# Performance work log

Hardware: AMD Instinct MI355X
Metric: run time of the kernel (lower is better)

Reference implementation:

```python
import jax, jax.numpy as jnp
import numpy as np

# Face order: [+x, -x, +y, -y, +z, -z]

def _rot(v, face):
    # v: (B,3,nx,ny,nz) -> rotate into face-normal frame (rotate_vec_to_face_normal)
    vx, vy, vz = v[:, 0], v[:, 1], v[:, 2]
    if face == 0:  # +x
        return jnp.stack([vx, vy, vz], axis=1)
    if face == 1:  # -x
        return jnp.stack([-vx, vy, vz], axis=1)
    if face == 2:  # +y
        return jnp.stack([vy, vx, vz], axis=1)
    if face == 3:  # -y
        return jnp.stack([-vy, vx, vz], axis=1)
    if face == 4:  # +z
        return jnp.stack([vz, vx, vy], axis=1)
    return jnp.stack([-vz, vx, vy], axis=1)  # -z


def _neighbors(f):
    # f: (B,C,nx,ny,nz); x,y periodic, z non-periodic (zero pad)
    dst_px = jnp.roll(f, -1, axis=-3)
    dst_mx = jnp.roll(f, 1, axis=-3)
    dst_py = jnp.roll(f, -1, axis=-2)
    dst_my = jnp.roll(f, 1, axis=-2)
    z = jnp.zeros_like(f[..., :1])
    dst_pz = jnp.concatenate([f[..., 1:], z], axis=-1)
    dst_mz = jnp.concatenate([z, f[..., :-1]], axis=-1)
    return [dst_px, dst_mx, dst_py, dst_my, dst_pz, dst_mz]


def setup_inputs() -> dict:
    key = jax.random.key(0)
    ks = jax.random.split(key, 10)
    B, s, nx, ny, nz, H = 2, 8, 48, 48, 48, 64
    in_ch = 2 * (s + 5)   # 26
    out_ch = 4 + 5 * s    # 44
    counts = jax.random.uniform(ks[0], (B, s, nx, ny, nz), jnp.float32)
    momentum = jax.random.normal(ks[1], (B, 3, nx, ny, nz), jnp.float32)
    ke = jax.random.uniform(ks[2], (B, 1, nx, ny, nz), jnp.float32)
    order = jax.random.uniform(ks[3], (B, 1, nx, ny, nz), jnp.float32)

    def lin(k, o, i):
        k1, k2 = jax.random.split(k)
        lim = 1.0 / np.sqrt(i)
        W = jax.random.uniform(k1, (o, i), jnp.float32, -lim, lim)
        b = jax.random.uniform(k2, (o,), jnp.float32, -lim, lim)
        return W, b

    W1, b1 = lin(ks[4], H, in_ch)
    W2, b2 = lin(ks[5], H, H)
    W3, b3 = lin(ks[6], out_ch, H)
    return dict(counts=counts, momentum=momentum, ke=ke, order=order,
                W1=W1, b1=b1, W2=W2, b2=b2, W3=W3, b3=b3)


def reference(counts, momentum, ke, order, W1, b1, W2, b2, W3, b3):
    s = counts.shape[1]
    # state.as_features(): channel concat [counts(S), momentum(3), ke(1), order(1)]
    features = jnp.concatenate([counts, momentum, ke, order], axis=1)
    dsts = _neighbors(features)
    src_counts = features[:, :s]
    src_mom = features[:, s:s + 3]
    src_rest = features[:, s + 3:s + 5]  # ke, order
    face_in = []
    for face in range(6):
        d = dsts[face]
        face_in.append(jnp.concatenate([
            src_counts, _rot(src_mom, face), src_rest,
            d[:, :s], _rot(d[:, s:s + 3], face), d[:, s + 3:s + 5]], axis=1))
    x = jnp.stack(face_in, axis=1)  # (B,6,in_ch,nx,ny,nz)
    # 1x1 Conv3d == channel matmul (the permutes in the original cancel for pointwise convs)
    bc = lambda b: b[None, None, :, None, None, None]
    h = jax.nn.silu(jnp.einsum('oc,bfcxyz->bfoxyz', W1, x) + bc(b1))
    h = jax.nn.silu(jnp.einsum('oc,bfcxyz->bfoxyz', W2, h) + bc(b2))
    out = jnp.einsum('oc,bfcxyz->bfoxyz', W3, h) + bc(b3)
    B, F, _, nx, ny, nz = out.shape
    force_momentum_flux = out[:, :, 0:3]                       # (B,6,3,nx,ny,nz)
    force_ke_flux = jax.nn.softplus(out[:, :, 3])              # (B,6,nx,ny,nz)
    atom_flux = jax.nn.softplus(out[:, :, 4:4 + s])            # (B,6,S,nx,ny,nz)
    material_momentum_flux = out[:, :, 4 + s:4 + 4 * s].reshape(B, F, s, 3, nx, ny, nz)
    material_ke_flux = jax.nn.softplus(out[:, :, 4 + 4 * s:4 + 5 * s])
    return (atom_flux, material_momentum_flux, material_ke_flux,
            force_momentum_flux, force_ke_flux)
```

## Files before the change

### kernel.cpp

```cpp
#include <hip/hip_runtime.h>

typedef unsigned short u16;
typedef unsigned int   u32;
typedef __attribute__((ext_vector_type(8))) short bf16x8;
typedef __attribute__((ext_vector_type(4))) float f32x4;
typedef union { u32 w[4]; bf16x8 v; } bfpack;

#define NV 110592

#define OFF_A  0u
#define OFF_MM (96u*NV)
#define OFF_MK (384u*NV)
#define OFF_FM (480u*NV)
#define OFF_FK (516u*NV)

__device__ __forceinline__ u16 f2bf(float f) {
  u32 u = __float_as_uint(f);
  u += 0x7FFFu + ((u >> 16) & 1u);
  return (u16)(u >> 16);
}
__device__ __forceinline__ u32 cvtpk(float a, float b) {
  u32 r; asm("v_cvt_pk_bf16_f32 %0, %1, %2" : "=v"(r) : "v"(a), "v"(b)); return r;
}
__device__ __forceinline__ float silu_f(float x) {
  float s = __builtin_amdgcn_rcpf(1.0f + __builtin_amdgcn_exp2f(-1.44269504089f * x));
  return x * s;
}
__device__ __forceinline__ float softplus_f(float x) {
  float e = __builtin_amdgcn_exp2f(-1.44269504089f * fabsf(x));
  return fmaxf(x, 0.0f) + 0.69314718056f * __builtin_amdgcn_logf(1.0f + e);
}
__device__ __forceinline__ int chmap(int r, int m) {
  return ((r >> 1) << 5) + ((m >> 2) << 3) + ((r & 1) << 2) + (m & 3);
}

__global__ void pack_weights(const float* __restrict__ W1, const float* __restrict__ b1,
                             const float* __restrict__ W2, const float* __restrict__ b2,
                             const float* __restrict__ W3, const float* __restrict__ b3,
                             u16* __restrict__ wsA, float* __restrict__ wsB)
{
  const int l  = threadIdx.x;
  const int m  = l & 15;
  const int hq = l >> 4;
  const int f  = blockIdx.x;

  if (f < 24) {
    const int face = f >> 2, r = f & 3;
    const int row  = chmap(r, m);
    const int   slot_tbl[6][3] = {{0,1,2},{0,1,2},{1,0,2},{1,0,2},{1,2,0},{1,2,0}};
    const float sign_tbl[6][3] = {{1,1,1},{-1,1,1},{1,1,1},{1,-1,1},{1,1,1},{1,1,-1}};
    #pragma unroll
    for (int j = 0; j < 8; ++j) {
      const int k = hq * 8 + j;
      float v;
      if      (k < 8)   v = W1[row * 26 + k];
      else if (k < 11)  { int cm = k - 8;  v = sign_tbl[face][cm] * W1[row * 26 + 8  + slot_tbl[face][cm]]; }
      else if (k == 11) v = W1[row * 26 + 11];
      else if (k == 12) v = W1[row * 26 + 12];
      else if (k == 13) v = b1[row];
      else if (k < 16)  v = 0.0f;
      else if (k < 24)  v = W1[row * 26 + 13 + (k - 16)];
      else if (k < 27)  { int cm = k - 24; v = sign_tbl[face][cm] * W1[row * 26 + 21 + slot_tbl[face][cm]]; }
      else if (k == 27) v = W1[row * 26 + 24];
      else if (k == 28) v = W1[row * 26 + 25];
      else              v = 0.0f;
      wsA[(f * 64 + l) * 8 + j] = f2bf(v);
    }
  } else if (f < 32) {
    const int r = (f - 24) >> 1, t = (f - 24) & 1;
    const int row = chmap(r, m);
    #pragma unroll
    for (int j = 0; j < 8; ++j) {
      const int k = t * 32 + hq * 8 + j;
      wsA[(f * 64 + l) * 8 + j] = f2bf(W2[row * 64 + k]);
    }
  } else if (f < 38) {
    const int r = (f - 32) >> 1, t = (f - 32) & 1;
    const int row = r * 16 + m;
    #pragma unroll
    for (int j = 0; j < 8; ++j) {
      const int k = t * 32 + hq * 8 + j;
      float v = (row < 44) ? W3[row * 64 + k] : 0.0f;
      wsA[(f * 64 + l) * 8 + j] = f2bf(v);
    }
  } else if (f == 38) {
    #pragma unroll
    for (int s = 0; s < 16; ++s) {
      const int r = s >> 2, jj = s & 3;
      wsB[s * 64 + l] = b2[chmap(r, hq * 4 + jj)];
    }
  } else {
    #pragma unroll
    for (int s = 0; s < 12; ++s) {
      const int r = s >> 2, jj = s & 3;
      const int o = r * 16 + hq * 4 + jj;
      wsB[(16 + s) * 64 + l] = (o < 44) ? b3[o] : 0.0f;
    }
  }
}

__global__ __launch_bounds__(256, 2) void fused_mlp(
    const float* __restrict__ counts, const float* __restrict__ momentum,
    const float* __restrict__ ke, const float* __restrict__ order,
    const u16* __restrict__ wsA, const float* __restrict__ wsB,
    float* __restrict__ out)
{
  __shared__ u16 xs[2][64 * 40];
  const int tid = threadIdx.x;
  const int ln  = tid & 63;
  const int wv  = tid >> 6;
  const int q   = ln >> 4;
  const int nn  = ln & 15;
  const int b   = blockIdx.y;
  const int vbase = blockIdx.x * 64;
  const int v   = vbase + ln;

  const int z = v % 48;
  const int rr = v / 48;
  const int y = rr % 48;
  const int x = rr / 48;
  int dvs[6];
  dvs[0] = v + ((x == 47) ? -108288 : 2304);
  dvs[1] = v + ((x == 0)  ?  108288 : -2304);
  dvs[2] = v + ((y == 47) ? -2256   : 48);
  dvs[3] = v + ((y == 0)  ?  2256   : -48);
  dvs[4] = v + 1;
  dvs[5] = v - 1;
  const bool val4 = (z != 47), val5 = (z != 0);

  const float* dchp[4];
  #pragma unroll
  for (int i = 0; i < 4; ++i) {
    const int c = 4 * wv + i;
    const float* p = nullptr;
    if      (c < 8)   p = counts   + ((size_t)b * 8 + c) * NV;
    else if (c < 11)  p = momentum + ((size_t)b * 3 + (c - 8)) * NV;
    else if (c == 11) p = ke    + (size_t)b * NV;
    else if (c == 12) p = order + (size_t)b * NV;
    dchp[i] = p;
  }

  const bf16x8* wsAf = (const bf16x8*)wsA;
  bf16x8 A2[4][2], A3[3][2];
  #pragma unroll
  for (int r = 0; r < 4; ++r)
    #pragma unroll
    for (int t = 0; t < 2; ++t) A2[r][t] = wsAf[(24 + r * 2 + t) * 64 + ln];
  #pragma unroll
  for (int r = 0; r < 3; ++r)
    #pragma unroll
    for (int t = 0; t < 2; ++t) A3[r][t] = wsAf[(32 + r * 2 + t) * 64 + ln];
  float b2v[16], b3v[12];
  #pragma unroll
  for (int s = 0; s < 16; ++s) b2v[s] = wsB[s * 64 + ln];
  #pragma unroll
  for (int s = 0; s < 12; ++s) b3v[s] = wsB[(16 + s) * 64 + ln];

  bf16x8 A1buf[2][4];
  #pragma unroll
  for (int r = 0; r < 4; ++r) A1buf[0][r] = wsAf[r * 64 + ln];

  u32 cb[12], fsv[12];
  u32 spmask = 0, vmask = 0;
  #pragma unroll
  for (int r3 = 0; r3 < 3; ++r3) {
    #pragma unroll
    for (int jj = 0; jj < 4; ++jj) {
      const int slot = r3 * 4 + jj;
      const int o = r3 * 16 + q * 4 + jj;
      u32 c0 = 0, f0 = 0; bool sp = false, va = true;
      if (o < 3)       { c0 = OFF_FM + (u32)o * NV;        f0 = 3u * NV; }
      else if (o == 3) { c0 = OFF_FK;                      f0 = 1u * NV; sp = true; }
      else if (o < 12) { c0 = OFF_A  + (u32)(o - 4) * NV;  f0 = 8u * NV; sp = true; }
      else if (o < 36) { c0 = OFF_MM + (u32)(o - 12) * NV; f0 = 24u * NV; }
      else if (o < 44) { c0 = OFF_MK + (u32)(o - 36) * NV; f0 = 8u * NV; sp = true; }
      else va = false;
      cb[slot] = c0; fsv[slot] = f0;
      if (sp) spmask |= (1u << slot);
      if (va) vmask  |= (1u << slot);
    }
  }

  {
    float sv[4];
    #pragma unroll
    for (int i = 0; i < 4; ++i) {
      const int k = 4 * wv + i;
      sv[i] = dchp[i] ? dchp[i][v] : ((k == 13) ? 1.0f : 0.0f);
    }
    const uint2 pk = make_uint2(cvtpk(sv[0], sv[1]), cvtpk(sv[2], sv[3]));
    *(uint2*)(&xs[0][ln * 40 + wv * 4]) = pk;
    *(uint2*)(&xs[1][ln * 40 + wv * 4]) = pk;
  }
  {
    float d0[4];
    #pragma unroll
    for (int i = 0; i < 4; ++i) d0[i] = dchp[i] ? dchp[i][dvs[0]] : 0.0f;
    *(uint2*)(&xs[0][ln * 40 + 16 + wv * 4]) =
        make_uint2(cvtpk(d0[0], d0[1]), cvtpk(d0[2], d0[3]));
  }

  __syncthreads();

  const u32 vg = (u32)(vbase + wv * 16 + nn);
  const u32 b6 = (u32)(b * 6);

  #pragma unroll
  for (int f = 0; f < 6; ++f) {
    float ndv[4] = {0.0f, 0.0f, 0.0f, 0.0f};
    if (f < 5) {
      const int nf = f + 1;
      const bool nval = (nf == 4) ? val4 : ((nf == 5) ? val5 : true);
      #pragma unroll
      for (int i = 0; i < 4; ++i)
        if (dchp[i] && nval) ndv[i] = dchp[i][dvs[nf]];
    }
    if (f < 5) {
      #pragma unroll
      for (int r = 0; r < 4; ++r)
        A1buf[(f + 1) & 1][r] = wsAf[((f + 1) * 4 + r) * 64 + ln];
    }

    const u16* xrow = &xs[f & 1][(wv * 16 + nn) * 40];
    const bf16x8 B1 = *(const bf16x8*)(xrow + q * 8);

    const f32x4 zf = {0.0f, 0.0f, 0.0f, 0.0f};
    f32x4 acc1[4];
    #pragma unroll
    for (int r = 0; r < 4; ++r)
      acc1[r] = __builtin_amdgcn_mfma_f32_16x16x32_bf16(A1buf[f & 1][r], B1, zf, 0, 0, 0);

    bfpack B2p[2];
    #pragma unroll
    for (int t = 0; t < 2; ++t) {
      B2p[t].w[0] = cvtpk(silu_f(acc1[t*2][0]),   silu_f(acc1[t*2][1]));
      B2p[t].w[1] = cvtpk(silu_f(acc1[t*2][2]),   silu_f(acc1[t*2][3]));
      B2p[t].w[2] = cvtpk(silu_f(acc1[t*2+1][0]), silu_f(acc1[t*2+1][1]));
      B2p[t].w[3] = cvtpk(silu_f(acc1[t*2+1][2]), silu_f(acc1[t*2+1][3]));
    }

    f32x4 acc2[4];
    #pragma unroll
    for (int r = 0; r < 4; ++r) {
      f32x4 ci = {b2v[4*r+0], b2v[4*r+1], b2v[4*r+2], b2v[4*r+3]};
      acc2[r] = __builtin_amdgcn_mfma_f32_16x16x32_bf16(A2[r][0], B2p[0].v, ci, 0, 0, 0);
      acc2[r] = __builtin_amdgcn_mfma_f32_16x16x32_bf16(A2[r][1], B2p[1].v, acc2[r], 0, 0, 0);
    }

    bfpack B3p[2];
    #pragma unroll
    for (int t = 0; t < 2; ++t) {
      B3p[t].w[0] = cvtpk(silu_f(acc2[t*2][0]),   silu_f(acc2[t*2][1]));
      B3p[t].w[1] = cvtpk(silu_f(acc2[t*2][2]),   silu_f(acc2[t*2][3]));
      B3p[t].w[2] = cvtpk(silu_f(acc2[t*2+1][0]), silu_f(acc2[t*2+1][1]));
      B3p[t].w[3] = cvtpk(silu_f(acc2[t*2+1][2]), silu_f(acc2[t*2+1][3]));
    }

    f32x4 acc3[3];
    #pragma unroll
    for (int r = 0; r < 3; ++r) {
      f32x4 ci = {b3v[4*r+0], b3v[4*r+1], b3v[4*r+2], b3v[4*r+3]};
      acc3[r] = __builtin_amdgcn_mfma_f32_16x16x32_bf16(A3[r][0], B3p[0].v, ci, 0, 0, 0);
      acc3[r] = __builtin_amdgcn_mfma_f32_16x16x32_bf16(A3[r][1], B3p[1].v, acc3[r], 0, 0, 0);
    }

    const u32 b6f = b6 + (u32)f;
    #pragma unroll
    for (int r3 = 0; r3 < 3; ++r3) {
      #pragma unroll
      for (int jj = 0; jj < 4; ++jj) {
        const int slot = r3 * 4 + jj;
        float val = acc3[r3][jj];
        float res = ((spmask >> slot) & 1u) ? softplus_f(val) : val;
        if ((vmask >> slot) & 1u)
          out[cb[slot] + b6f * fsv[slot] + vg] = res;
      }
    }

    if (f < 5) {
      *(uint2*)(&xs[(f + 1) & 1][ln * 40 + 16 + wv * 4]) =
          make_uint2(cvtpk(ndv[0], ndv[1]), cvtpk(ndv[2], ndv[3]));
    }
    __syncthreads();
  }
}

extern "C" void kernel_launch(void* const* d_in, const int* in_sizes, int n_in,
                              void* d_out, int out_size, void* d_ws, size_t ws_size,
                              hipStream_t stream)
{
  const float* counts   = (const float*)d_in[0];
  const float* momentum = (const float*)d_in[1];
  const float* ke       = (const float*)d_in[2];
  const float* order    = (const float*)d_in[3];
  const float* W1 = (const float*)d_in[4];
  const float* b1 = (const float*)d_in[5];
  const float* W2 = (const float*)d_in[6];
  const float* b2 = (const float*)d_in[7];
  const float* W3 = (const float*)d_in[8];
  const float* b3 = (const float*)d_in[9];

  u16*   wsA = (u16*)d_ws;
  float* wsB = (float*)((char*)d_ws + 38 * 64 * 8 * sizeof(u16));

  pack_weights<<<dim3(40), dim3(64), 0, stream>>>(W1, b1, W2, b2, W3, b3, wsA, wsB);
  fused_mlp<<<dim3(1728, 2), dim3(256), 0, stream>>>(counts, momentum, ke, order,
                                                     wsA, wsB, (float*)d_out);
}
```

Before: 309.0 us.

## Load MFMA B operand directly from global per lane, drop LDS staging and barriers

Each lane now loads exactly the 8 input channels its MFMA B-fragment needs (source or neighbor, counts or momentum/ke/order) straight from global memory into registers, replacing the shared-memory staging buffer and the per-face __syncthreads. Output addressing is precomputed per slot and incremented by the face stride. This removes LDS traffic and block-wide barriers but duplicates some global loads: source channels are reloaded each face (cache hits) and padding lanes issue redundant loads.

```diff
diff --git a/kernel.cpp b/kernel.cpp
--- a/kernel.cpp
+++ b/kernel.cpp
@@ -105,39 +105,47 @@
     const u16* __restrict__ wsA, const float* __restrict__ wsB,
     float* __restrict__ out)
 {
-  __shared__ u16 xs[2][64 * 40];
   const int tid = threadIdx.x;
   const int ln  = tid & 63;
   const int wv  = tid >> 6;
   const int q   = ln >> 4;
   const int nn  = ln & 15;
   const int b   = blockIdx.y;
-  const int vbase = blockIdx.x * 64;
-  const int v   = vbase + ln;
-
-  const int z = v % 48;
-  const int rr = v / 48;
-  const int y = rr % 48;
-  const int x = rr / 48;
+  const int v16 = blockIdx.x * 64 + wv * 16 + nn;
+
+  const int z  = v16 % 48;
+  const int rr = v16 / 48;
+  const int y  = rr % 48;
+  const int x  = rr / 48;
+
+  const bool isdst = (q >= 2);
+  const bool qodd  = (q & 1);
+  const float bias5 = (q == 1) ? 1.0f : 0.0f;
+  const bool inval4 = isdst && (z == 47);
+  const bool inval5 = isdst && (z == 0);
+
   int dvs[6];
-  dvs[0] = v + ((x == 47) ? -108288 : 2304);
-  dvs[1] = v + ((x == 0)  ?  108288 : -2304);
-  dvs[2] = v + ((y == 47) ? -2256   : 48);
-  dvs[3] = v + ((y == 0)  ?  2256   : -48);
-  dvs[4] = v + 1;
-  dvs[5] = v - 1;
-  const bool val4 = (z != 47), val5 = (z != 0);
-
-  const float* dchp[4];
-  #pragma unroll
-  for (int i = 0; i < 4; ++i) {
-    const int c = 4 * wv + i;
-    const float* p = nullptr;
-    if      (c < 8)   p = counts   + ((size_t)b * 8 + c) * NV;
-    else if (c < 11)  p = momentum + ((size_t)b * 3 + (c - 8)) * NV;
-    else if (c == 11) p = ke    + (size_t)b * NV;
-    else if (c == 12) p = order + (size_t)b * NV;
-    dchp[i] = p;
+  dvs[0] = isdst ? (v16 + ((x == 47) ? -108288 : 2304)) : v16;
+  dvs[1] = isdst ? (v16 + ((x == 0)  ?  108288 : -2304)) : v16;
+  dvs[2] = isdst ? (v16 + ((y == 47) ? -2256   : 48))    : v16;
+  dvs[3] = isdst ? (v16 + ((y == 0)  ?  2256   : -48))   : v16;
+  dvs[4] = (isdst && z != 47) ? v16 + 1 : v16;
+  dvs[5] = (isdst && z != 0)  ? v16 - 1 : v16;
+
+  const float* BP[8];
+  #pragma unroll
+  for (int j = 0; j < 8; ++j) {
+    const float* p;
+    if (!qodd) {
+      p = counts + ((size_t)b * 8 + j) * NV;
+    } else {
+      const int c = 8 + j;
+      if      (c < 11)  p = momentum + ((size_t)b * 3 + (c - 8)) * NV;
+      else if (c == 11) p = ke    + (size_t)b * NV;
+      else if (c == 12) p = order + (size_t)b * NV;
+      else              p = ke    + (size_t)b * NV;
+    }
+    BP[j] = p;
   }
 
   const bf16x8* wsAf = (const bf16x8*)wsA;
@@ -156,11 +164,7 @@
   #pragma unroll
   for (int s = 0; s < 12; ++s) b3v[s] = wsB[(16 + s) * 64 + ln];
 
-  bf16x8 A1buf[2][4];
-  #pragma unroll
-  for (int r = 0; r < 4; ++r) A1buf[0][r] = wsAf[r * 64 + ln];
-
-  u32 cb[12], fsv[12];
+  u32 off[12], fsv[12];
   u32 spmask = 0, vmask = 0;
   #pragma unroll
   for (int r3 = 0; r3 < 3; ++r3) {
@@ -175,60 +179,43 @@
       else if (o < 36) { c0 = OFF_MM + (u32)(o - 12) * NV; f0 = 24u * NV; }
       else if (o < 44) { c0 = OFF_MK + (u32)(o - 36) * NV; f0 = 8u * NV; sp = true; }
       else va = false;
-      cb[slot] = c0; fsv[slot] = f0;
+      off[slot] = c0 + (u32)(b * 6) * f0 + (u32)v16;
+      fsv[slot] = f0;
       if (sp) spmask |= (1u << slot);
       if (va) vmask  |= (1u << slot);
     }
   }
 
-  {
-    float sv[4];
-    #pragma unroll
-    for (int i = 0; i < 4; ++i) {
-      const int k = 4 * wv + i;
-      sv[i] = dchp[i] ? dchp[i][v] : ((k == 13) ? 1.0f : 0.0f);
-    }
-    const uint2 pk = make_uint2(cvtpk(sv[0], sv[1]), cvtpk(sv[2], sv[3]));
-    *(uint2*)(&xs[0][ln * 40 + wv * 4]) = pk;
-    *(uint2*)(&xs[1][ln * 40 + wv * 4]) = pk;
-  }
-  {
-    float d0[4];
-    #pragma unroll
-    for (int i = 0; i < 4; ++i) d0[i] = dchp[i] ? dchp[i][dvs[0]] : 0.0f;
-    *(uint2*)(&xs[0][ln * 40 + 16 + wv * 4]) =
-        make_uint2(cvtpk(d0[0], d0[1]), cvtpk(d0[2], d0[3]));
-  }
-
-  __syncthreads();
-
-  const u32 vg = (u32)(vbase + wv * 16 + nn);
-  const u32 b6 = (u32)(b * 6);
+  float cur[8], nxt[8];
+  bf16x8 A1c[4], A1n[4];
+  #pragma unroll
+  for (int j = 0; j < 8; ++j) cur[j] = BP[j][dvs[0]];
+  cur[5] = qodd ? bias5 : cur[5];
+  cur[6] = qodd ? 0.0f : cur[6];
+  cur[7] = qodd ? 0.0f : cur[7];
+  #pragma unroll
+  for (int r = 0; r < 4; ++r) A1c[r] = wsAf[r * 64 + ln];
 
   #pragma unroll
   for (int f = 0; f < 6; ++f) {
-    float ndv[4] = {0.0f, 0.0f, 0.0f, 0.0f};
     if (f < 5) {
-      const int nf = f + 1;
-      const bool nval = (nf == 4) ? val4 : ((nf == 5) ? val5 : true);
-      #pragma unroll
-      for (int i = 0; i < 4; ++i)
-        if (dchp[i] && nval) ndv[i] = dchp[i][dvs[nf]];
-    }
-    if (f < 5) {
-      #pragma unroll
-      for (int r = 0; r < 4; ++r)
-        A1buf[(f + 1) & 1][r] = wsAf[((f + 1) * 4 + r) * 64 + ln];
-    }
-
-    const u16* xrow = &xs[f & 1][(wv * 16 + nn) * 40];
-    const bf16x8 B1 = *(const bf16x8*)(xrow + q * 8);
+      #pragma unroll
+      for (int j = 0; j < 8; ++j) nxt[j] = BP[j][dvs[f + 1]];
+      #pragma unroll
+      for (int r = 0; r < 4; ++r) A1n[r] = wsAf[((f + 1) * 4 + r) * 64 + ln];
+    }
+
+    bfpack B1;
+    B1.w[0] = cvtpk(cur[0], cur[1]);
+    B1.w[1] = cvtpk(cur[2], cur[3]);
+    B1.w[2] = cvtpk(cur[4], cur[5]);
+    B1.w[3] = cvtpk(cur[6], cur[7]);
 
     const f32x4 zf = {0.0f, 0.0f, 0.0f, 0.0f};
     f32x4 acc1[4];
     #pragma unroll
     for (int r = 0; r < 4; ++r)
-      acc1[r] = __builtin_amdgcn_mfma_f32_16x16x32_bf16(A1buf[f & 1][r], B1, zf, 0, 0, 0);
+      acc1[r] = __builtin_amdgcn_mfma_f32_16x16x32_bf16(A1c[r], B1.v, zf, 0, 0, 0);
 
     bfpack B2p[2];
     #pragma unroll
@@ -264,7 +251,6 @@
       acc3[r] = __builtin_amdgcn_mfma_f32_16x16x32_bf16(A3[r][1], B3p[1].v, acc3[r], 0, 0, 0);
     }
 
-    const u32 b6f = b6 + (u32)f;
     #pragma unroll
     for (int r3 = 0; r3 < 3; ++r3) {
       #pragma unroll
@@ -273,15 +259,23 @@
         float val = acc3[r3][jj];
         float res = ((spmask >> slot) & 1u) ? softplus_f(val) : val;
         if ((vmask >> slot) & 1u)
-          out[cb[slot] + b6f * fsv[slot] + vg] = res;
+          out[off[slot]] = res;
+        off[slot] += fsv[slot];
       }
     }
 
     if (f < 5) {
-      *(uint2*)(&xs[(f + 1) & 1][ln * 40 + 16 + wv * 4]) =
-          make_uint2(cvtpk(ndv[0], ndv[1]), cvtpk(ndv[2], ndv[3]));
-    }
-    __syncthreads();
+      const bool inv = ((f + 1) == 4) ? inval4 : (((f + 1) == 5) ? inval5 : false);
+      #pragma unroll
+      for (int j = 0; j < 8; ++j) nxt[j] = inv ? 0.0f : nxt[j];
+      nxt[5] = qodd ? bias5 : nxt[5];
+      nxt[6] = qodd ? 0.0f : nxt[6];
+      nxt[7] = qodd ? 0.0f : nxt[7];
+      #pragma unroll
+      for (int j = 0; j < 8; ++j) cur[j] = nxt[j];
+      #pragma unroll
+      for (int r = 0; r < 4; ++r) A1c[r] = A1n[r];
+    }
   }
 }
 
```

Result: faster. 297.9 us (-3.6%).
